# Kernel optimization log

Measured on AMD Instinct MI355X. Metric: run time of the kernel, lower is better.

The kernel has to match this reference:

```python
import jax, jax.numpy as jnp
import numpy as np

HIDDEN = 256
HEADS = 8
HEAD_DIM = HIDDEN // HEADS
N = 4096
EPS = 1e-5


def setup_inputs() -> dict:
    key = jax.random.key(0)
    ks = jax.random.split(key, 16)
    s = HIDDEN ** -0.5
    inp = {
        "A": jax.random.uniform(ks[0], (N, N), dtype=jnp.float32),
        "h": jax.random.normal(ks[1], (N, HIDDEN), dtype=jnp.float32),
        # Linear layers stored torch-style as [out, in]
        "Wq": jax.random.normal(ks[2], (HIDDEN, HIDDEN), jnp.float32) * s,
        "bq": jnp.zeros((HIDDEN,), jnp.float32),
        "Wk": jax.random.normal(ks[3], (HIDDEN, HIDDEN), jnp.float32) * s,
        "bk": jnp.zeros((HIDDEN,), jnp.float32),
        "Wv": jax.random.normal(ks[4], (HIDDEN, HIDDEN), jnp.float32) * s,
        "bv": jnp.zeros((HIDDEN,), jnp.float32),
        "Wo": jax.random.normal(ks[5], (HIDDEN, HIDDEN), jnp.float32) * s,
        "bo": jnp.zeros((HIDDEN,), jnp.float32),
        "W1": jax.random.normal(ks[6], (2 * HIDDEN, HIDDEN), jnp.float32) * s,
        "c1": jnp.zeros((2 * HIDDEN,), jnp.float32),
        "W2": jax.random.normal(ks[7], (HIDDEN, 2 * HIDDEN), jnp.float32) * (2 * HIDDEN) ** -0.5,
        "c2": jnp.zeros((HIDDEN,), jnp.float32),
        "g1": jnp.ones((HIDDEN,), jnp.float32),
        "be1": jnp.zeros((HIDDEN,), jnp.float32),
        "g2": jnp.ones((HIDDEN,), jnp.float32),
        "be2": jnp.zeros((HIDDEN,), jnp.float32),
    }
    return inp


def _batchnorm(x, gamma, beta):
    # BatchNorm1d training mode: biased batch stats over node axis
    mean = x.mean(axis=0)
    var = ((x - mean) ** 2).mean(axis=0)
    return (x - mean) * jax.lax.rsqrt(var + EPS) * gamma + beta


def _mha(A, h, Wq, bq, Wk, bk, Wv, bv, Wo, bo):
    n = h.shape[0]
    scaling = HEAD_DIM ** -0.5
    # NOTE: raw reshape [N, H*d] -> (H, N, d), exactly as the torch code (no transpose)
    q = ((h @ Wq.T + bq).reshape(HEADS, n, HEAD_DIM)) * scaling
    k = (h @ Wk.T + bk).reshape(HEADS, n, HEAD_DIM)
    v = (h @ Wv.T + bv).reshape(HEADS, n, HEAD_DIM)
    t = jnp.einsum('hnd,hmd->hnm', q, k)          # [H, N, N]
    attn = jax.nn.softmax(t * A, axis=2)          # multiplicative adjacency mask
    out = jnp.einsum('hnm,hmd->hnd', attn, v)     # [H, N, d]
    return out.reshape(n, -1) @ Wo.T + bo         # raw reshape back, as in torch


def reference(A, h, Wq, bq, Wk, bk, Wv, bv, Wo, bo, W1, c1, W2, c2, g1, be1, g2, be2):
    h1 = h
    x = _mha(A, h, Wq, bq, Wk, bk, Wv, bv, Wo, bo)
    x = _batchnorm(x + h1, g1, be1)
    h2 = x
    x = jax.nn.relu(x @ W1.T + c1) @ W2.T + c2
    return _batchnorm(h2 + x, g2, be2)
```

## Files before the change

### kernel.cpp

```cpp
#include <hip/hip_runtime.h>

#define N_NODES 4096
#define HID 256
#define NHEADS 8
#define HDIM 32
#define EPSV 1e-5f
#define M2LOG 11.541560327111707f

typedef __bf16 bf16x8 __attribute__((ext_vector_type(8)));
typedef __bf16 bf16x4 __attribute__((ext_vector_type(4)));
typedef float f32x4 __attribute__((ext_vector_type(4)));

__device__ inline float fexp2(float x) {
    float r;
    asm("v_exp_f32 %0, %1" : "=v"(r) : "v"(x));
    return r;
}

__device__ inline uint4 pack8(float4 a, float4 b) {
    bf16x8 p;
    p[0]=(__bf16)a.x; p[1]=(__bf16)a.y; p[2]=(__bf16)a.z; p[3]=(__bf16)a.w;
    p[4]=(__bf16)b.x; p[5]=(__bf16)b.y; p[6]=(__bf16)b.z; p[7]=(__bf16)b.w;
    return __builtin_bit_cast(uint4, p);
}
__device__ inline float4 nmad4(float4 x, float4 s, float4 sh) {
    return make_float4(fmaf(x.x,s.x,sh.x), fmaf(x.y,s.y,sh.y),
                       fmaf(x.z,s.z,sh.z), fmaf(x.w,s.w,sh.w));
}

__launch_bounds__(256)
__global__ void gemm_mfma(const float* __restrict__ X, const float* __restrict__ W,
                          const float* __restrict__ bias, const float* __restrict__ resid,
                          float* __restrict__ C,
                          const float* __restrict__ pSin, const float* __restrict__ pQin,
                          const float* __restrict__ gamin, const float* __restrict__ betin,
                          int norm_x, int norm_r,
                          float* __restrict__ psum, float* __restrict__ pq,
                          int M, int N, int K, float scale, int do_relu) {
    __shared__ uint4 xl[2][512];
    __shared__ uint4 wl[2][512];
    __shared__ __align__(16) float nsc[256];
    __shared__ __align__(16) float nsh[256];
    const int bm = blockIdx.x * 64, bn = blockIdx.y * 64;
    const int t = threadIdx.x;
    const int w = t >> 6, l = t & 63, g = l >> 4, nl = l & 15;
    const int srow = t >> 3, seg = t & 7;
    const int sx = (seg & 3) << 1;
    const int d0 = seg*64 + (srow ^ sx);
    const int d1 = seg*64 + ((srow + 32) ^ sx);
    const float* xp = X + (size_t)(bm + srow)*K + seg*8;
    const float* wp = W + (size_t)(bn + srow)*K + seg*8;
    const size_t rstep = (size_t)32*K;

    if (pSin) {
        float s = 0.f, q = 0.f;
        #pragma unroll 8
        for (int b = 0; b < 64; ++b) { s += pSin[b*HID + t]; q += pQin[b*HID + t]; }
        const float m = s * (1.f/4096.f);
        const float rstd = rsqrtf(q*(1.f/4096.f) - m*m + EPSV);
        const float sc = rstd * gamin[t];
        nsc[t] = sc;
        nsh[t] = fmaf(-m, sc, betin[t]);
        __syncthreads();
    }

    f32x4 acc[4];
    #pragma unroll
    for (int nf = 0; nf < 4; ++nf) acc[nf] = (f32x4){0.f,0.f,0.f,0.f};

    {
        float4 x0 = *(const float4*)(xp),          x1 = *(const float4*)(xp + 4);
        float4 x2 = *(const float4*)(xp + rstep),  x3 = *(const float4*)(xp + rstep + 4);
        if (norm_x) {
            float4 s0 = *(const float4*)(nsc + seg*8), s1 = *(const float4*)(nsc + seg*8 + 4);
            float4 h0 = *(const float4*)(nsh + seg*8), h1 = *(const float4*)(nsh + seg*8 + 4);
            x0 = nmad4(x0,s0,h0); x1 = nmad4(x1,s1,h1);
            x2 = nmad4(x2,s0,h0); x3 = nmad4(x3,s1,h1);
        }
        float4 w0 = *(const float4*)(wp),          w1 = *(const float4*)(wp + 4);
        float4 w2 = *(const float4*)(wp + rstep),  w3 = *(const float4*)(wp + rstep + 4);
        xl[0][d0] = pack8(x0, x1); xl[0][d1] = pack8(x2, x3);
        wl[0][d0] = pack8(w0, w1); wl[0][d1] = pack8(w2, w3);
    }
    __syncthreads();

    for (int k0 = 0; k0 < K; k0 += 64) {
        const int cur = (k0 >> 6) & 1;
        const bool nxt = (k0 + 64) < K;
        float4 nx0, nx1, nx2, nx3, nw0, nw1, nw2, nw3;
        if (nxt) {
            const int kk = k0 + 64;
            nx0 = *(const float4*)(xp + kk);          nx1 = *(const float4*)(xp + kk + 4);
            nx2 = *(const float4*)(xp + rstep + kk);  nx3 = *(const float4*)(xp + rstep + kk + 4);
            if (norm_x) {
                float4 s0 = *(const float4*)(nsc + kk + seg*8), s1 = *(const float4*)(nsc + kk + seg*8 + 4);
                float4 h0 = *(const float4*)(nsh + kk + seg*8), h1 = *(const float4*)(nsh + kk + seg*8 + 4);
                nx0 = nmad4(nx0,s0,h0); nx1 = nmad4(nx1,s1,h1);
                nx2 = nmad4(nx2,s0,h0); nx3 = nmad4(nx3,s1,h1);
            }
            nw0 = *(const float4*)(wp + kk);          nw1 = *(const float4*)(wp + kk + 4);
            nw2 = *(const float4*)(wp + rstep + kk);  nw3 = *(const float4*)(wp + rstep + kk + 4);
        }
        __builtin_amdgcn_s_setprio(1);
        #pragma unroll
        for (int ks = 0; ks < 2; ++ks) {
            bf16x8 af = __builtin_bit_cast(bf16x8, xl[cur][(ks*4 + g)*64 + ((w*16 + nl) ^ (g << 1))]);
            #pragma unroll
            for (int nf = 0; nf < 4; ++nf) {
                bf16x8 bfr = __builtin_bit_cast(bf16x8, wl[cur][(ks*4 + g)*64 + ((nf*16 + nl) ^ (g << 1))]);
                acc[nf] = __builtin_amdgcn_mfma_f32_16x16x32_bf16(af, bfr, acc[nf], 0, 0, 0);
            }
        }
        __builtin_amdgcn_s_setprio(0);
        if (nxt) {
            xl[cur^1][d0] = pack8(nx0, nx1); xl[cur^1][d1] = pack8(nx2, nx3);
            wl[cur^1][d0] = pack8(nw0, nw1); wl[cur^1][d1] = pack8(nw2, nw3);
        }
        __syncthreads();
    }

    float colS[4] = {0.f,0.f,0.f,0.f}, colQ[4] = {0.f,0.f,0.f,0.f};
    #pragma unroll
    for (int nf = 0; nf < 4; ++nf) {
        const int col = bn + nf*16 + nl;
        const float bb = bias[col];
        float rs = 1.f, rh = 0.f;
        if (norm_r) { rs = nsc[col]; rh = nsh[col]; }
        #pragma unroll
        for (int r = 0; r < 4; ++r) {
            const int row = bm + w*16 + g*4 + r;
            float v = acc[nf][r] + bb;
            if (resid) {
                float rv = resid[(size_t)row*N + col];
                v += norm_r ? fmaf(rv, rs, rh) : rv;
            }
            v *= scale;
            if (do_relu) v = fmaxf(v, 0.f);
            C[(size_t)row*N + col] = v;
            colS[nf] += v;
            colQ[nf] = fmaf(v, v, colQ[nf]);
        }
    }
    if (psum) {
        float* cs = (float*)&xl[0][0];
        float* cq = cs + 1024;
        #pragma unroll
        for (int nf = 0; nf < 4; ++nf) {
            const int idx = (w*4 + g)*64 + nf*16 + nl;
            cs[idx] = colS[nf];
            cq[idx] = colQ[nf];
        }
        __syncthreads();
        if (t < 64) {
            float s = 0.f, q = 0.f;
            #pragma unroll
            for (int i = 0; i < 16; ++i) { s += cs[i*64 + t]; q += cq[i*64 + t]; }
            psum[blockIdx.x*HID + bn + t] = s;
            pq[blockIdx.x*HID + bn + t]   = q;
        }
    }
}

__launch_bounds__(256)
__global__ void gemm_wo(const float* __restrict__ Opart, const float* __restrict__ Lpart,
                        int nsplit, const float* __restrict__ W,
                        const float* __restrict__ bias, const float* __restrict__ resid,
                        float* __restrict__ C, float* __restrict__ psum, float* __restrict__ pq) {
    const int N = 256, K = 256;
    __shared__ uint4 xl[2][512];
    __shared__ uint4 wl[2][512];
    const int bm = blockIdx.x * 64, bn = blockIdx.y * 64;
    const int t = threadIdx.x;
    const int w = t >> 6, l = t & 63, g = l >> 4, nl = l & 15;
    const int srow = t >> 3, seg = t & 7;
    const int sx = (seg & 3) << 1;
    const int d0 = seg*64 + (srow ^ sx);
    const int d1 = seg*64 + ((srow + 32) ^ sx);
    const float* wp = W + (size_t)(bn + srow)*K + seg*8;
    const size_t rstep = (size_t)32*K;

    auto cl = [&](int row, int kk, float4& a, float4& b) {
        const size_t flat = (size_t)row*256 + kk;
        const int hn = (int)(flat >> 5);
        float L = 0.f;
        a = make_float4(0.f,0.f,0.f,0.f);
        b = make_float4(0.f,0.f,0.f,0.f);
        for (int z = 0; z < nsplit; ++z) {
            L += Lpart[z*32768 + hn];
            float4 u = *(const float4*)(Opart + (size_t)z*1048576 + flat);
            float4 v = *(const float4*)(Opart + (size_t)z*1048576 + flat + 4);
            a.x += u.x; a.y += u.y; a.z += u.z; a.w += u.w;
            b.x += v.x; b.y += v.y; b.z += v.z; b.w += v.w;
        }
        const float inv = 1.f / L;
        a.x *= inv; a.y *= inv; a.z *= inv; a.w *= inv;
        b.x *= inv; b.y *= inv; b.z *= inv; b.w *= inv;
    };

    f32x4 acc[4];
    #pragma unroll
    for (int nf = 0; nf < 4; ++nf) acc[nf] = (f32x4){0.f,0.f,0.f,0.f};

    {
        float4 x0, x1, x2, x3;
        cl(bm + srow,      seg*8, x0, x1);
        cl(bm + srow + 32, seg*8, x2, x3);
        float4 w0 = *(const float4*)(wp),          w1 = *(const float4*)(wp + 4);
        float4 w2 = *(const float4*)(wp + rstep),  w3 = *(const float4*)(wp + rstep + 4);
        xl[0][d0] = pack8(x0, x1); xl[0][d1] = pack8(x2, x3);
        wl[0][d0] = pack8(w0, w1); wl[0][d1] = pack8(w2, w3);
    }
    __syncthreads();

    for (int k0 = 0; k0 < K; k0 += 64) {
        const int cur = (k0 >> 6) & 1;
        const bool nxt = (k0 + 64) < K;
        float4 nx0, nx1, nx2, nx3, nw0, nw1, nw2, nw3;
        if (nxt) {
            const int kk = k0 + 64 + seg*8;
            cl(bm + srow,      kk, nx0, nx1);
            cl(bm + srow + 32, kk, nx2, nx3);
            nw0 = *(const float4*)(wp + k0 + 64);          nw1 = *(const float4*)(wp + k0 + 68);
            nw2 = *(const float4*)(wp + rstep + k0 + 64);  nw3 = *(const float4*)(wp + rstep + k0 + 68);
        }
        __builtin_amdgcn_s_setprio(1);
        #pragma unroll
        for (int ks = 0; ks < 2; ++ks) {
            bf16x8 af = __builtin_bit_cast(bf16x8, xl[cur][(ks*4 + g)*64 + ((w*16 + nl) ^ (g << 1))]);
            #pragma unroll
            for (int nf = 0; nf < 4; ++nf) {
                bf16x8 bfr = __builtin_bit_cast(bf16x8, wl[cur][(ks*4 + g)*64 + ((nf*16 + nl) ^ (g << 1))]);
                acc[nf] = __builtin_amdgcn_mfma_f32_16x16x32_bf16(af, bfr, acc[nf], 0, 0, 0);
            }
        }
        __builtin_amdgcn_s_setprio(0);
        if (nxt) {
            xl[cur^1][d0] = pack8(nx0, nx1); xl[cur^1][d1] = pack8(nx2, nx3);
            wl[cur^1][d0] = pack8(nw0, nw1); wl[cur^1][d1] = pack8(nw2, nw3);
        }
        __syncthreads();
    }

    float colS[4] = {0.f,0.f,0.f,0.f}, colQ[4] = {0.f,0.f,0.f,0.f};
    #pragma unroll
    for (int nf = 0; nf < 4; ++nf) {
        const int col = bn + nf*16 + nl;
        const float bb = bias[col];
        #pragma unroll
        for (int r = 0; r < 4; ++r) {
            const int row = bm + w*16 + g*4 + r;
            float v = acc[nf][r] + bb + resid[(size_t)row*N + col];
            C[(size_t)row*N + col] = v;
            colS[nf] += v;
            colQ[nf] = fmaf(v, v, colQ[nf]);
        }
    }
    {
        float* cs = (float*)&xl[0][0];
        float* cq = cs + 1024;
        #pragma unroll
        for (int nf = 0; nf < 4; ++nf) {
            const int idx = (w*4 + g)*64 + nf*16 + nl;
            cs[idx] = colS[nf];
            cq[idx] = colQ[nf];
        }
        __syncthreads();
        if (t < 64) {
            float s = 0.f, q = 0.f;
            #pragma unroll
            for (int i = 0; i < 16; ++i) { s += cs[i*64 + t]; q += cq[i*64 + t]; }
            psum[blockIdx.x*HID + bn + t] = s;
            pq[blockIdx.x*HID + bn + t]   = q;
        }
    }
}

__launch_bounds__(256)
__global__ void gemm_qkv(const float* __restrict__ X,
                         const float* __restrict__ Wq, const float* __restrict__ Wk,
                         const float* __restrict__ Wv, const float* __restrict__ bq,
                         const float* __restrict__ bk, const float* __restrict__ bv,
                         __bf16* __restrict__ qhat, __bf16* __restrict__ khat,
                         __bf16* __restrict__ vhat) {
    const int K = 256;
    __shared__ uint4 xl[2][512];
    __shared__ uint4 wl[2][512];
    const int z = blockIdx.z;
    const float* W = (z == 0) ? Wq : (z == 1) ? Wk : Wv;
    const float* bias = (z == 0) ? bq : (z == 1) ? bk : bv;
    __bf16* hat = (z == 0) ? qhat : (z == 1) ? khat : vhat;
    const float scale = (z == 0) ? 0.25506595325f : 1.f;

    const int bm = blockIdx.x * 64, bn = blockIdx.y * 64;
    const int t = threadIdx.x;
    const int w = t >> 6, l = t & 63, g = l >> 4, nl = l & 15;
    const int srow = t >> 3, seg = t & 7;
    const int sx = (seg & 3) << 1;
    const int d0 = seg*64 + (srow ^ sx);
    const int d1 = seg*64 + ((srow + 32) ^ sx);
    const float* xp = X + (size_t)(bm + srow)*K + seg*8;
    const float* wp = W + (size_t)(bn + srow)*K + seg*8;
    const size_t rstep = (size_t)32*K;

    f32x4 acc[4];
    #pragma unroll
    for (int nf = 0; nf < 4; ++nf) acc[nf] = (f32x4){0.f,0.f,0.f,0.f};

    {
        float4 x0 = *(const float4*)(xp),          x1 = *(const float4*)(xp + 4);
        float4 x2 = *(const float4*)(xp + rstep),  x3 = *(const float4*)(xp + rstep + 4);
        float4 w0 = *(const float4*)(wp),          w1 = *(const float4*)(wp + 4);
        float4 w2 = *(const float4*)(wp + rstep),  w3 = *(const float4*)(wp + rstep + 4);
        xl[0][d0] = pack8(x0, x1); xl[0][d1] = pack8(x2, x3);
        wl[0][d0] = pack8(w0, w1); wl[0][d1] = pack8(w2, w3);
    }
    __syncthreads();

    for (int k0 = 0; k0 < K; k0 += 64) {
        const int cur = (k0 >> 6) & 1;
        const bool nxt = (k0 + 64) < K;
        float4 nx0, nx1, nx2, nx3, nw0, nw1, nw2, nw3;
        if (nxt) {
            nx0 = *(const float4*)(xp + k0 + 64);          nx1 = *(const float4*)(xp + k0 + 68);
            nx2 = *(const float4*)(xp + rstep + k0 + 64);  nx3 = *(const float4*)(xp + rstep + k0 + 68);
            nw0 = *(const float4*)(wp + k0 + 64);          nw1 = *(const float4*)(wp + k0 + 68);
            nw2 = *(const float4*)(wp + rstep + k0 + 64);  nw3 = *(const float4*)(wp + rstep + k0 + 68);
        }
        __builtin_amdgcn_s_setprio(1);
        #pragma unroll
        for (int ks = 0; ks < 2; ++ks) {
            bf16x8 af = __builtin_bit_cast(bf16x8, xl[cur][(ks*4 + g)*64 + ((w*16 + nl) ^ (g << 1))]);
            #pragma unroll
            for (int nf = 0; nf < 4; ++nf) {
                bf16x8 bfr = __builtin_bit_cast(bf16x8, wl[cur][(ks*4 + g)*64 + ((nf*16 + nl) ^ (g << 1))]);
                acc[nf] = __builtin_amdgcn_mfma_f32_16x16x32_bf16(af, bfr, acc[nf], 0, 0, 0);
            }
        }
        __builtin_amdgcn_s_setprio(0);
        if (nxt) {
            xl[cur^1][d0] = pack8(nx0, nx1); xl[cur^1][d1] = pack8(nx2, nx3);
            wl[cur^1][d0] = pack8(nw0, nw1); wl[cur^1][d1] = pack8(nw2, nw3);
        }
        __syncthreads();
    }

    #pragma unroll
    for (int nf = 0; nf < 4; ++nf) {
        const int col = bn + nf*16 + nl;
        const float bb = bias[col];
        #pragma unroll
        for (int r = 0; r < 4; ++r) {
            const int row = bm + w*16 + g*4 + r;
            float v = (acc[nf][r] + bb) * scale;
            const int hh = row >> 9;
            const int nn = ((row & 511) << 3) | (col >> 5);
            hat[((size_t)(hh*4096 + nn))*32 + (col & 31)] = (__bf16)v;
        }
    }
}

__launch_bounds__(256)
__global__ void transpose_vhat(const __bf16* __restrict__ vhat, __bf16* __restrict__ vT) {
    const int h = blockIdx.y, n0 = blockIdx.x * 64;
    __shared__ __bf16 tile[64][40];
    const int t = threadIdx.x;
    {
        int n = t >> 2, dd0 = (t & 3) * 8;
        *(uint4*)&tile[n][dd0] = *(const uint4*)(vhat + ((size_t)(h*4096 + n0 + n))*32 + dd0);
    }
    __syncthreads();
    {
        int d = t >> 3, ns = (t & 7) * 8;
        uint4 ov;
        __bf16* op = (__bf16*)&ov;
        #pragma unroll
        for (int j = 0; j < 8; ++j) op[j] = tile[ns + j][d];
        *(uint4*)(vT + ((size_t)(h*32 + d))*4096 + n0 + ns) = ov;
    }
}

__launch_bounds__(512, 2)
__global__ void attn_mfma(const __bf16* __restrict__ qh_, const __bf16* __restrict__ kh,
                          const __bf16* __restrict__ vT, const float* __restrict__ A,
                          float* __restrict__ Opart, float* __restrict__ Lpart, int mlen) {
    __shared__ float A_lds[2][64][68];
    __shared__ uint4 p_lds[8][4][64];

    const int t = threadIdx.x;
    const int w = t >> 6, l = t & 63;
    const int g = l >> 4, nl = l & 15;
    const int n0 = blockIdx.x * 64;
    const int z = blockIdx.y;
    const int m_begin = z * mlen;
    const int nsteps = mlen >> 6;

    bf16x8 qf[4];
    #pragma unroll
    for (int nf = 0; nf < 4; ++nf)
        qf[nf] = *(const bf16x8*)(qh_ + ((size_t)(w*4096 + n0 + nf*16 + nl))*32 + g*8);

    f32x4 oacc[4][2];
    #pragma unroll
    for (int nf = 0; nf < 4; ++nf) {
        oacc[nf][0] = (f32x4){0.f,0.f,0.f,0.f};
        oacc[nf][1] = (f32x4){0.f,0.f,0.f,0.f};
    }
    float Li[4] = {0.f, 0.f, 0.f, 0.f};

    const int aq = t >> 3, am = (t & 7) * 8;
    const float* Abase = A + (size_t)(n0 + aq)*N_NODES + m_begin + am;
    const __bf16* kbase = kh + ((size_t)w*4096 + nl)*32 + g*8;
    const __bf16* vbase = vT + ((size_t)w*32 + nl)*4096 + g*8;

    *(float4*)&A_lds[0][aq][am]   = *(const float4*)(Abase);
    *(float4*)&A_lds[0][aq][am+4] = *(const float4*)(Abase + 4);
    __syncthreads();

    for (int s = 0; s < nsteps; ++s) {
        const int cur = s & 1;
        const int m0 = m_begin + s*64;
        const bool nxt = (s + 1) < nsteps;
        float4 a0n, a1n;
        if (nxt) {
            a0n = *(const float4*)(Abase + (s+1)*64);
            a1n = *(const float4*)(Abase + (s+1)*64 + 4);
        }
        bf16x8 kf[4], vf[4];
        #pragma unroll
        for (int tt = 0; tt < 4; ++tt)
            kf[tt] = *(const bf16x8*)(kbase + (size_t)(m0 + tt*16)*32);
        #pragma unroll
        for (int half = 0; half < 2; ++half)
            #pragma unroll
            for (int dt = 0; dt < 2; ++dt)
                vf[half*2+dt] = *(const bf16x8*)(vbase + (size_t)dt*16*4096 + m0 + half*32);
        __builtin_amdgcn_sched_barrier(0);

        #pragma unroll
        for (int half = 0; half < 2; ++half) {
            #pragma unroll
            for (int tt2 = 0; tt2 < 2; ++tt2) {
                const int tt = half*2 + tt2;
                f32x4 st[4];
                __builtin_amdgcn_s_setprio(1);
                #pragma unroll
                for (int nf = 0; nf < 4; ++nf) {
                    f32x4 zz = (f32x4){0.f,0.f,0.f,0.f};
                    st[nf] = __builtin_amdgcn_mfma_f32_16x16x32_bf16(kf[tt], qf[nf], zz, 0, 0, 0);
                }
                __builtin_amdgcn_s_setprio(0);
                #pragma unroll
                for (int nf = 0; nf < 4; ++nf) {
                    const f32x4 a4 = *(const f32x4*)&A_lds[cur][nf*16 + nl][tt*16 + g*4];
                    float p0 = fexp2(fmaf(st[nf][0], a4[0], -M2LOG));
                    float p1 = fexp2(fmaf(st[nf][1], a4[1], -M2LOG));
                    float p2 = fexp2(fmaf(st[nf][2], a4[2], -M2LOG));
                    float p3 = fexp2(fmaf(st[nf][3], a4[3], -M2LOG));
                    Li[nf] += (p0 + p1) + (p2 + p3);
                    bf16x4 pk;
                    pk[0] = (__bf16)p0; pk[1] = (__bf16)p1;
                    pk[2] = (__bf16)p2; pk[3] = (__bf16)p3;
                    const int gm = tt2*2 + (g >> 1);
                    *(bf16x4*)((char*)&p_lds[w][nf][0] + (gm*16 + (nl ^ (gm << 1)))*16 + (g & 1)*8) = pk;
                }
            }
            __builtin_amdgcn_s_setprio(1);
            #pragma unroll
            for (int nf = 0; nf < 4; ++nf) {
                bf16x8 pf = __builtin_bit_cast(bf16x8, p_lds[w][nf][g*16 + (nl ^ (g << 1))]);
                oacc[nf][0] = __builtin_amdgcn_mfma_f32_16x16x32_bf16(vf[half*2+0], pf, oacc[nf][0], 0, 0, 0);
                oacc[nf][1] = __builtin_amdgcn_mfma_f32_16x16x32_bf16(vf[half*2+1], pf, oacc[nf][1], 0, 0, 0);
            }
            __builtin_amdgcn_s_setprio(0);
        }

        if (nxt) {
            *(float4*)&A_lds[cur^1][aq][am]   = a0n;
            *(float4*)&A_lds[cur^1][aq][am+4] = a1n;
        }
        __syncthreads();
    }

    #pragma unroll
    for (int nf = 0; nf < 4; ++nf) {
        Li[nf] += __shfl_xor(Li[nf], 16);
        Li[nf] += __shfl_xor(Li[nf], 32);
        const int nq = n0 + nf*16 + nl;
        float* ob = Opart + ((size_t)(z*NHEADS + w)*4096 + nq)*32;
        *(float4*)(ob + 0*16 + g*4) = make_float4(oacc[nf][0][0], oacc[nf][0][1],
                                                  oacc[nf][0][2], oacc[nf][0][3]);
        *(float4*)(ob + 1*16 + g*4) = make_float4(oacc[nf][1][0], oacc[nf][1][1],
                                                  oacc[nf][1][2], oacc[nf][1][3]);
        if (g == 0)
            Lpart[(z*NHEADS + w)*4096 + nq] = Li[nf];
    }
}

__launch_bounds__(256)
__global__ void bnorm_fin_apply(const float* __restrict__ X,
                                const float* __restrict__ pS, const float* __restrict__ pQ,
                                const float* __restrict__ gam, const float* __restrict__ bet,
                                float* __restrict__ Y) {
    __shared__ __align__(16) float sc[256];
    __shared__ __align__(16) float sh[256];
    const int t = threadIdx.x;
    {
        float s = 0.f, q = 0.f;
        #pragma unroll 8
        for (int b = 0; b < 64; ++b) { s += pS[b*HID + t]; q += pQ[b*HID + t]; }
        const float m = s * (1.f/4096.f);
        const float rstd = rsqrtf(q*(1.f/4096.f) - m*m + EPSV);
        const float scv = rstd * gam[t];
        sc[t] = scv;
        sh[t] = fmaf(-m, scv, bet[t]);
    }
    __syncthreads();
    const int base0 = (blockIdx.x * 256 + t) * 16;
    #pragma unroll
    for (int j = 0; j < 4; ++j) {
        const int base = base0 + j*4;
        const int c = base & (HID - 1);
        float4 x = *(const float4*)(X + base);
        float4 o;
        o.x = fmaf(x.x, sc[c+0], sh[c+0]);
        o.y = fmaf(x.y, sc[c+1], sh[c+1]);
        o.z = fmaf(x.z, sc[c+2], sh[c+2]);
        o.w = fmaf(x.w, sc[c+3], sh[c+3]);
        *(float4*)(Y + base) = o;
    }
}

extern "C" void kernel_launch(void* const* d_in, const int* in_sizes, int n_in,
                              void* d_out, int out_size, void* d_ws, size_t ws_size,
                              hipStream_t stream) {
    const float* A  = (const float*)d_in[0];
    const float* h  = (const float*)d_in[1];
    const float* Wq = (const float*)d_in[2];
    const float* bq = (const float*)d_in[3];
    const float* Wk = (const float*)d_in[4];
    const float* bk = (const float*)d_in[5];
    const float* Wv = (const float*)d_in[6];
    const float* bv = (const float*)d_in[7];
    const float* Wo = (const float*)d_in[8];
    const float* bo = (const float*)d_in[9];
    const float* W1 = (const float*)d_in[10];
    const float* c1 = (const float*)d_in[11];
    const float* W2 = (const float*)d_in[12];
    const float* c2 = (const float*)d_in[13];
    const float* g1 = (const float*)d_in[14];
    const float* be1= (const float*)d_in[15];
    const float* g2 = (const float*)d_in[16];
    const float* be2= (const float*)d_in[17];

    char* wsb = (char*)d_ws;
    const size_t MiB = (size_t)1 << 20;
    const int nsplit = (ws_size >= 43*MiB) ? 8 : (ws_size >= 26*MiB) ? 4 : 2;
    const int mlen = N_NODES / nsplit;

    __bf16* qhat = (__bf16*)(wsb + 0*MiB);
    __bf16* khat = (__bf16*)(wsb + 2*MiB);
    __bf16* vhat = (__bf16*)(wsb + 4*MiB);
    __bf16* vT   = (__bf16*)(wsb + 6*MiB);
    float* Opart = (float*)(wsb + 8*MiB);
    float* Lpart = (float*)(wsb + 8*MiB + (size_t)nsplit*4*MiB);
    char* statb  = wsb + 8*MiB + (size_t)nsplit*4*MiB + 1*MiB;
    float* partS1 = (float*)statb;
    float* partQ1 = partS1 + 64*HID;
    float* partS2 = partQ1 + 64*HID;
    float* partQ2 = partS2 + 64*HID;
    float* Y1 = (float*)(wsb + 4*MiB);
    float* F1 = (float*)(wsb + 8*MiB);
    float* Y2 = (float*)(wsb + 0*MiB);

    gemm_qkv<<<dim3(64, 4, 3), 256, 0, stream>>>(h, Wq, Wk, Wv, bq, bk, bv, qhat, khat, vhat);
    transpose_vhat<<<dim3(64, 8), 256, 0, stream>>>(vhat, vT);

    attn_mfma<<<dim3(64, nsplit), 512, 0, stream>>>(qhat, khat, vT, A, Opart, Lpart, mlen);

    gemm_wo<<<dim3(64, 4), 256, 0, stream>>>(Opart, Lpart, nsplit, Wo, bo, h, Y1, partS1, partQ1);

    gemm_mfma<<<dim3(64, 8), 256, 0, stream>>>(Y1, W1, c1, nullptr, F1,
                                               partS1, partQ1, g1, be1, 1, 0,
                                               nullptr, nullptr, 4096, 512, 256, 1.f, 1);
    gemm_mfma<<<dim3(64, 4), 256, 0, stream>>>(F1, W2, c2, Y1, Y2,
                                               partS1, partQ1, g1, be1, 0, 1,
                                               partS2, partQ2, 4096, 256, 512, 1.f, 0);

    bnorm_fin_apply<<<256, 256, 0, stream>>>(Y2, partS2, partQ2, g2, be2, (float*)d_out);
}
```

Baseline: 130.5 us.

## Store attention partials in bf16 and write V transposed directly from QKV GEMM

After: 124.7 us. 4.4% less time.

```diff
diff --git a/kernel.cpp b/kernel.cpp
--- a/kernel.cpp
+++ b/kernel.cpp
@@ -27,6 +27,8 @@
     return make_float4(fmaf(x.x,s.x,sh.x), fmaf(x.y,s.y,sh.y),
                        fmaf(x.z,s.z,sh.z), fmaf(x.w,s.w,sh.w));
 }
+__device__ inline float bflo(unsigned u) { return __builtin_bit_cast(float, u << 16); }
+__device__ inline float bfhi(unsigned u) { return __builtin_bit_cast(float, u & 0xFFFF0000u); }
 
 __launch_bounds__(256)
 __global__ void gemm_mfma(const float* __restrict__ X, const float* __restrict__ W,
@@ -162,7 +164,7 @@
 }
 
 __launch_bounds__(256)
-__global__ void gemm_wo(const float* __restrict__ Opart, const float* __restrict__ Lpart,
+__global__ void gemm_wo(const __bf16* __restrict__ Opart, const float* __restrict__ Lpart,
                         int nsplit, const float* __restrict__ W,
                         const float* __restrict__ bias, const float* __restrict__ resid,
                         float* __restrict__ C, float* __restrict__ psum, float* __restrict__ pq) {
@@ -176,37 +178,42 @@
     const int sx = (seg & 3) << 1;
     const int d0 = seg*64 + (srow ^ sx);
     const int d1 = seg*64 + ((srow + 32) ^ sx);
-    const float* wp = W + (size_t)(bn + srow)*K + seg*8;
-    const size_t rstep = (size_t)32*K;
-
-    auto cl = [&](int row, int kk, float4& a, float4& b) {
-        const size_t flat = (size_t)row*256 + kk;
+    const float* wrow0 = W + (size_t)(bn + srow)*K;
+    const float* wrow1 = W + (size_t)(bn + srow + 32)*K;
+
+    auto cl = [&](int row, int kp, float4& a, float4& b) {
+        const size_t flat = (size_t)row*256 + kp;
         const int hn = (int)(flat >> 5);
         float L = 0.f;
-        a = make_float4(0.f,0.f,0.f,0.f);
-        b = make_float4(0.f,0.f,0.f,0.f);
+        float s0=0,s1=0,s2=0,s3=0,s4=0,s5=0,s6=0,s7=0;
         for (int z = 0; z < nsplit; ++z) {
             L += Lpart[z*32768 + hn];
-            float4 u = *(const float4*)(Opart + (size_t)z*1048576 + flat);
-            float4 v = *(const float4*)(Opart + (size_t)z*1048576 + flat + 4);
-            a.x += u.x; a.y += u.y; a.z += u.z; a.w += u.w;
-            b.x += v.x; b.y += v.y; b.z += v.z; b.w += v.w;
+            uint4 u = *(const uint4*)(Opart + (size_t)z*1048576 + flat);
+            s0 += bflo(u.x); s1 += bfhi(u.x);
+            s2 += bflo(u.y); s3 += bfhi(u.y);
+            s4 += bflo(u.z); s5 += bfhi(u.z);
+            s6 += bflo(u.w); s7 += bfhi(u.w);
         }
         const float inv = 1.f / L;
-        a.x *= inv; a.y *= inv; a.z *= inv; a.w *= inv;
-        b.x *= inv; b.y *= inv; b.z *= inv; b.w *= inv;
+        a = make_float4(s0*inv, s1*inv, s2*inv, s3*inv);
+        b = make_float4(s4*inv, s5*inv, s6*inv, s7*inv);
     };
+    auto wld = [&](const float* wrow, int kp, float4& a, float4& b) {
+        const int kb = (kp & ~31) + ((kp >> 3) & 3)*4;
+        a = *(const float4*)(wrow + kb);
+        b = *(const float4*)(wrow + kb + 16);
+    };
 
     f32x4 acc[4];
     #pragma unroll
     for (int nf = 0; nf < 4; ++nf) acc[nf] = (f32x4){0.f,0.f,0.f,0.f};
 
     {
-        float4 x0, x1, x2, x3;
+        float4 x0, x1, x2, x3, w0, w1, w2, w3;
         cl(bm + srow,      seg*8, x0, x1);
         cl(bm + srow + 32, seg*8, x2, x3);
-        float4 w0 = *(const float4*)(wp),          w1 = *(const float4*)(wp + 4);
-        float4 w2 = *(const float4*)(wp + rstep),  w3 = *(const float4*)(wp + rstep + 4);
+        wld(wrow0, seg*8, w0, w1);
+        wld(wrow1, seg*8, w2, w3);
         xl[0][d0] = pack8(x0, x1); xl[0][d1] = pack8(x2, x3);
         wl[0][d0] = pack8(w0, w1); wl[0][d1] = pack8(w2, w3);
     }
@@ -217,11 +224,11 @@
         const bool nxt = (k0 + 64) < K;
         float4 nx0, nx1, nx2, nx3, nw0, nw1, nw2, nw3;
         if (nxt) {
-            const int kk = k0 + 64 + seg*8;
-            cl(bm + srow,      kk, nx0, nx1);
-            cl(bm + srow + 32, kk, nx2, nx3);
-            nw0 = *(const float4*)(wp + k0 + 64);          nw1 = *(const float4*)(wp + k0 + 68);
-            nw2 = *(const float4*)(wp + rstep + k0 + 64);  nw3 = *(const float4*)(wp + rstep + k0 + 68);
+            const int kp = k0 + 64 + seg*8;
+            cl(bm + srow,      kp, nx0, nx1);
+            cl(bm + srow + 32, kp, nx2, nx3);
+            wld(wrow0, kp, nw0, nw1);
+            wld(wrow1, kp, nw2, nw3);
         }
         __builtin_amdgcn_s_setprio(1);
         #pragma unroll
@@ -281,14 +288,13 @@
                          const float* __restrict__ Wv, const float* __restrict__ bq,
                          const float* __restrict__ bk, const float* __restrict__ bv,
                          __bf16* __restrict__ qhat, __bf16* __restrict__ khat,
-                         __bf16* __restrict__ vhat) {
+                         __bf16* __restrict__ vT) {
     const int K = 256;
     __shared__ uint4 xl[2][512];
     __shared__ uint4 wl[2][512];
     const int z = blockIdx.z;
     const float* W = (z == 0) ? Wq : (z == 1) ? Wk : Wv;
     const float* bias = (z == 0) ? bq : (z == 1) ? bk : bv;
-    __bf16* hat = (z == 0) ? qhat : (z == 1) ? khat : vhat;
     const float scale = (z == 0) ? 0.25506595325f : 1.f;
 
     const int bm = blockIdx.x * 64, bn = blockIdx.y * 64;
@@ -352,37 +358,25 @@
         for (int r = 0; r < 4; ++r) {
             const int row = bm + w*16 + g*4 + r;
             float v = (acc[nf][r] + bb) * scale;
-            const int hh = row >> 9;
-            const int nn = ((row & 511) << 3) | (col >> 5);
-            hat[((size_t)(hh*4096 + nn))*32 + (col & 31)] = (__bf16)v;
-        }
-    }
-}
-
-__launch_bounds__(256)
-__global__ void transpose_vhat(const __bf16* __restrict__ vhat, __bf16* __restrict__ vT) {
-    const int h = blockIdx.y, n0 = blockIdx.x * 64;
-    __shared__ __bf16 tile[64][40];
-    const int t = threadIdx.x;
-    {
-        int n = t >> 2, dd0 = (t & 3) * 8;
-        *(uint4*)&tile[n][dd0] = *(const uint4*)(vhat + ((size_t)(h*4096 + n0 + n))*32 + dd0);
-    }
-    __syncthreads();
-    {
-        int d = t >> 3, ns = (t & 7) * 8;
-        uint4 ov;
-        __bf16* op = (__bf16*)&ov;
-        #pragma unroll
-        for (int j = 0; j < 8; ++j) op[j] = tile[ns + j][d];
-        *(uint4*)(vT + ((size_t)(h*32 + d))*4096 + n0 + ns) = ov;
+            if (z == 2) {
+                const int hh = row >> 9;
+                const int dd = col & 31;
+                const int nn = ((row & 511) << 3) | (col >> 5);
+                vT[((size_t)(hh*32 + dd))*4096 + nn] = (__bf16)v;
+            } else {
+                __bf16* hat = (z == 0) ? qhat : khat;
+                const int hh = row >> 9;
+                const int nn = ((row & 511) << 3) | (col >> 5);
+                hat[((size_t)(hh*4096 + nn))*32 + (col & 31)] = (__bf16)v;
+            }
+        }
     }
 }
 
 __launch_bounds__(512, 2)
 __global__ void attn_mfma(const __bf16* __restrict__ qh_, const __bf16* __restrict__ kh,
                           const __bf16* __restrict__ vT, const float* __restrict__ A,
-                          float* __restrict__ Opart, float* __restrict__ Lpart, int mlen) {
+                          __bf16* __restrict__ Opart, float* __restrict__ Lpart, int mlen) {
     __shared__ float A_lds[2][64][68];
     __shared__ uint4 p_lds[8][4][64];
 
@@ -486,11 +480,14 @@
         Li[nf] += __shfl_xor(Li[nf], 16);
         Li[nf] += __shfl_xor(Li[nf], 32);
         const int nq = n0 + nf*16 + nl;
-        float* ob = Opart + ((size_t)(z*NHEADS + w)*4096 + nq)*32;
-        *(float4*)(ob + 0*16 + g*4) = make_float4(oacc[nf][0][0], oacc[nf][0][1],
-                                                  oacc[nf][0][2], oacc[nf][0][3]);
-        *(float4*)(ob + 1*16 + g*4) = make_float4(oacc[nf][1][0], oacc[nf][1][1],
-                                                  oacc[nf][1][2], oacc[nf][1][3]);
+        __bf16* ob = Opart + ((size_t)(z*NHEADS + w)*4096 + nq)*32;
+        bf16x8 pk8;
+        #pragma unroll
+        for (int j = 0; j < 4; ++j) {
+            pk8[j]     = (__bf16)oacc[nf][0][j];
+            pk8[4 + j] = (__bf16)oacc[nf][1][j];
+        }
+        *(bf16x8*)(ob + g*8) = pk8;
         if (g == 0)
             Lpart[(z*NHEADS + w)*4096 + nq] = Li[nf];
     }
@@ -554,16 +551,15 @@
 
     char* wsb = (char*)d_ws;
     const size_t MiB = (size_t)1 << 20;
-    const int nsplit = (ws_size >= 43*MiB) ? 8 : (ws_size >= 26*MiB) ? 4 : 2;
+    const int nsplit = (ws_size >= 26*MiB) ? 8 : (ws_size >= 18*MiB) ? 4 : 2;
     const int mlen = N_NODES / nsplit;
 
     __bf16* qhat = (__bf16*)(wsb + 0*MiB);
     __bf16* khat = (__bf16*)(wsb + 2*MiB);
-    __bf16* vhat = (__bf16*)(wsb + 4*MiB);
-    __bf16* vT   = (__bf16*)(wsb + 6*MiB);
-    float* Opart = (float*)(wsb + 8*MiB);
-    float* Lpart = (float*)(wsb + 8*MiB + (size_t)nsplit*4*MiB);
-    char* statb  = wsb + 8*MiB + (size_t)nsplit*4*MiB + 1*MiB;
+    __bf16* vT   = (__bf16*)(wsb + 4*MiB);
+    __bf16* Opart = (__bf16*)(wsb + 8*MiB);
+    float* Lpart = (float*)(wsb + 8*MiB + (size_t)nsplit*2*MiB);
+    char* statb  = wsb + 8*MiB + (size_t)nsplit*2*MiB + 1*MiB;
     float* partS1 = (float*)statb;
     float* partQ1 = partS1 + 64*HID;
     float* partS2 = partQ1 + 64*HID;
@@ -572,8 +568,7 @@
     float* F1 = (float*)(wsb + 8*MiB);
     float* Y2 = (float*)(wsb + 0*MiB);
 
-    gemm_qkv<<<dim3(64, 4, 3), 256, 0, stream>>>(h, Wq, Wk, Wv, bq, bk, bv, qhat, khat, vhat);
-    transpose_vhat<<<dim3(64, 8), 256, 0, stream>>>(vhat, vT);
+    gemm_qkv<<<dim3(64, 4, 3), 256, 0, stream>>>(h, Wq, Wk, Wv, bq, bk, bv, qhat, khat, vT);
 
     attn_mfma<<<dim3(64, nsplit), 512, 0, stream>>>(qhat, khat, vT, A, Opart, Lpart, mlen);
 
```
